# Kernel optimization log

Hardware: AMD Instinct MI355X
Metric: run time of the kernel (lower is better)

## Reference

```python
import jax, jax.numpy as jnp
import numpy as np


def setup_inputs() -> dict:
    key = jax.random.key(0)
    k1, k2 = jax.random.split(key)
    bg = jax.random.normal(k1, (1, 4, 32, 32, 32, 16), dtype=jnp.float32)
    gm = jax.random.uniform(k2, (1, 1, 128, 128, 128), dtype=jnp.float32)
    return {"bg": bg, "gm": gm}


def _prep(coord, size):
    # replicate boundary: clamp sample coords into [0, size-1]
    coord = jnp.clip(coord, 0.0, float(size - 1))
    i0f = jnp.floor(coord)
    frac = coord - i0f
    i0 = i0f.astype(jnp.int32)
    i1 = jnp.minimum(i0 + 1, size - 1)
    return i0, i1, frac


def reference(bg, gm):
    # bg: (n,c,h,w,d,up) 4D bilateral grid; gm: (n,1,gh,gw,gd) guidance volume
    n, c, h, w, d, up = bg.shape
    _, _, gh, gw, gd = gm.shape
    f32 = jnp.float32

    # voxel-space sample coordinates (module: hg/(h_img-1) * (h-1) etc.)
    x = jnp.arange(gh, dtype=f32) * (f32(h - 1) / f32(gh - 1))  # (gh,)
    y = jnp.arange(gw, dtype=f32) * (f32(w - 1) / f32(gw - 1))  # (gw,)
    z = jnp.arange(gd, dtype=f32) * (f32(d - 1) / f32(gd - 1))  # (gd,)
    t = gm[:, 0] * f32(up - 1)                                   # (n,gh,gw,gd)

    x0, x1, fx = _prep(x, h)
    y0, y1, fy = _prep(y, w)
    z0, z1, fz = _prep(z, d)
    t0, t1, ft = _prep(t, up)

    def opts(i0, i1, frac, shape):
        i0 = i0.reshape(shape); i1 = i1.reshape(shape); frac = frac.reshape(shape)
        return [(i0, 1.0 - frac), (i1, frac)]

    xo = opts(x0, x1, fx, (1, gh, 1, 1))
    yo = opts(y0, y1, fy, (1, 1, gw, 1))
    zo = opts(z0, z1, fz, (1, 1, 1, gd))
    to = [(t0, 1.0 - ft), (t1, ft)]  # already (n,gh,gw,gd)

    bidx = jnp.arange(n)[:, None, None, None]        # (n,1,1,1)
    bgc = jnp.moveaxis(bg, 1, -1)                    # (n,h,w,d,up,c)

    acc = jnp.zeros((n, gh, gw, gd, c), dtype=bg.dtype)
    # 2^4 = 16 corners of quadri-linear interpolation (grid_pull order=1)
    for ix, wx in xo:
        for iy, wy in yo:
            for iz, wz in zo:
                for it, wt in to:
                    vals = bgc[bidx, ix, iy, iz, it]         # (n,gh,gw,gd,c)
                    wgt = (wx * wy * wz * wt)[..., None]     # (n,gh,gw,gd,1)
                    acc = acc + vals * wgt
    return jnp.moveaxis(acc, -1, 1)                  # (n,c,gh,gw,gd)
```

## Files before the change

kernel.cpp:

```cpp
#include <hip/hip_runtime.h>
#include <hip/hip_fp16.h>


#define S_ (31.0f / 127.0f)
#define CH_STRIDE 524288
#define TOTAL 2097152

#define NX 4
#define NY 4
#define NZ 10
#define NNODES (NX * NY * NZ)
#define NODE_DW 68
#define LDS_DW (NNODES * NODE_DW)

#define PK(x, y) __builtin_bit_cast(float, __floats2half2_rn((x), (y)))
#define H2(f) __builtin_bit_cast(__half2, f)

typedef float vf4 __attribute__((ext_vector_type(4)));

__device__ __forceinline__ void nt_store4(float* p, float a, float b, float c, float d) {
    vf4 v; v.x = a; v.y = b; v.z = c; v.w = d;
    __builtin_nontemporal_store(v, (vf4*)p);
}

__global__ __launch_bounds__(512, 6) void bgrid_slice_v14(
    const float* __restrict__ bg,
    const float* __restrict__ gm,
    float* __restrict__ out)
{
    __shared__ __align__(16) float lds[LDS_DW];

    const int tid = threadIdx.x;
    const int b = blockIdx.x;
    const int tile = ((b & 7) << 7) + (b >> 3);
    const int bk = tile & 3;
    const int bj = (tile >> 2) & 15;
    const int bi = tile >> 6;

    const int i0 = bi * 8, j0 = bj * 8, k0 = bk * 32;
    const int x_base = (int)((float)i0 * S_);
    const int y_base = (int)((float)j0 * S_);
    const int z_base = (int)((float)k0 * S_);

    const int kq = tid & 7;
    const int lj = (tid >> 3) & 7;
    const int li = tid >> 6;
    const int i = i0 + li, j = j0 + lj;
    const int kk = k0 + (kq << 2);
    const int idx = (i << 14) | (j << 7) | kk;
    const vf4 g4v = __builtin_nontemporal_load((const vf4*)&gm[idx]);
    float4 g4; g4.x = g4v.x; g4.y = g4v.y; g4.z = g4v.z; g4.w = g4v.w;

    #pragma unroll
    for (int it = 0; it < 2; ++it) {
        const int q = tid + (it << 9);
        if (q < 640) {
            const int s4 = q & 3;
            const int node = q >> 2;
            const int a = node / 40;
            const int rem = node - a * 40;
            const int bb = rem / 10;
            const int cz = rem - bb * 10;
            const int gx = min(x_base + a, 31);
            const int gy = min(y_base + bb, 31);
            const int gz = min(z_base + cz, 31);
            const int gbase = (((gx * 32 + gy) * 32 + gz) << 4) + (s4 << 2);

            const float4 L0 = *(const float4*)&bg[gbase];
            const float4 L1 = *(const float4*)&bg[gbase + CH_STRIDE];
            const float4 L2 = *(const float4*)&bg[gbase + 2 * CH_STRIDE];
            const float4 L3 = *(const float4*)&bg[gbase + 3 * CH_STRIDE];

            float2 p0, p1, p2, p3;
            p0.x = PK(L0.x, L1.x); p0.y = PK(L2.x, L3.x);
            p1.x = PK(L0.y, L1.y); p1.y = PK(L2.y, L3.y);
            p2.x = PK(L0.z, L1.z); p2.y = PK(L2.z, L3.z);
            p3.x = PK(L0.w, L1.w); p3.y = PK(L2.w, L3.w);

            const int s0 = node * NODE_DW + (s4 << 4);
            float4 w;
            w.x = p0.x; w.y = p0.y; w.z = p1.x; w.w = p1.y;
            *(float4*)&lds[s0] = w;
            w.x = p1.x; w.y = p1.y; w.z = p2.x; w.w = p2.y;
            *(float4*)&lds[s0 + 4] = w;
            w.x = p2.x; w.y = p2.y; w.z = p3.x; w.w = p3.y;
            *(float4*)&lds[s0 + 8] = w;
            if (s4 < 3) *(float2*)&lds[s0 + 12] = p3;
            if (s4 > 0) *(float2*)&lds[s0 - 2]  = p0;
        }
    }
    __syncthreads();

    const float xf = fminf((float)i * S_, 31.0f);
    const float yf = fminf((float)j * S_, 31.0f);
    const int x0g = (int)xf; const float fx = xf - (float)x0g;
    const int y0g = (int)yf; const float fy = yf - (float)y0g;
    const int xi0 = x0g - x_base, xi1 = min(x0g + 1, 31) - x_base;
    const int yi0 = y0g - y_base, yi1 = min(y0g + 1, 31) - y_base;

    const int AX0 = xi0 * (NY * NZ * NODE_DW);
    const int AX1 = xi1 * (NY * NZ * NODE_DW);
    const int BY0 = yi0 * (NZ * NODE_DW);
    const int BY1 = yi1 * (NZ * NODE_DW);

    const float wx1 = fx, wx0 = 1.0f - fx;
    const float wy1 = fy, wy0 = 1.0f - fy;
    const __half2 W00 = __float2half2_rn(wx0 * wy0);
    const __half2 W01 = __float2half2_rn(wx0 * wy1);
    const __half2 W10 = __float2half2_rn(wx1 * wy0);
    const __half2 W11 = __float2half2_rn(wx1 * wy1);

    float o0[4], o1[4], o2[4], o3[4];

#pragma unroll
    for (int v = 0; v < 4; ++v) {
        const float g = (v == 0) ? g4.x : (v == 1) ? g4.y : (v == 2) ? g4.z : g4.w;
        float t = fminf(fmaxf(g * 15.0f, 0.0f), 15.0f);
        const int t0 = min((int)t, 14);
        const float ft = t - (float)t0;
        const __half2 ft2 = __float2half2_rn(ft);

        const float zf = fminf((float)(kk + v) * S_, 31.0f);
        const int z0g = (int)zf;
        const float fz = zf - (float)z0g;
        const int zi0 = z0g - z_base;
        const int zi1 = min(z0g + 1, 31) - z_base;
        const __half2 fz2 = __float2half2_rn(fz);

        const int CZ0 = zi0 * NODE_DW + (t0 << 2);
        const int CZ1 = zi1 * NODE_DW + (t0 << 2);

        const float4 a00 = *(const float4*)&lds[AX0 + BY0 + CZ0];
        const float4 a01 = *(const float4*)&lds[AX0 + BY1 + CZ0];
        const float4 a10 = *(const float4*)&lds[AX1 + BY0 + CZ0];
        const float4 a11 = *(const float4*)&lds[AX1 + BY1 + CZ0];
        const float4 b00 = *(const float4*)&lds[AX0 + BY0 + CZ1];
        const float4 b01 = *(const float4*)&lds[AX0 + BY1 + CZ1];
        const float4 b10 = *(const float4*)&lds[AX1 + BY0 + CZ1];
        const float4 b11 = *(const float4*)&lds[AX1 + BY1 + CZ1];

        __half2 Plo01 = __hmul2(W00, H2(a00.x));
        __half2 Plo23 = __hmul2(W00, H2(a00.y));
        __half2 Phi01 = __hmul2(W00, H2(a00.z));
        __half2 Phi23 = __hmul2(W00, H2(a00.w));
        Plo01 = __hfma2(W01, H2(a01.x), Plo01);
        Plo23 = __hfma2(W01, H2(a01.y), Plo23);
        Phi01 = __hfma2(W01, H2(a01.z), Phi01);
        Phi23 = __hfma2(W01, H2(a01.w), Phi23);
        Plo01 = __hfma2(W10, H2(a10.x), Plo01);
        Plo23 = __hfma2(W10, H2(a10.y), Plo23);
        Phi01 = __hfma2(W10, H2(a10.z), Phi01);
        Phi23 = __hfma2(W10, H2(a10.w), Phi23);
        Plo01 = __hfma2(W11, H2(a11.x), Plo01);
        Plo23 = __hfma2(W11, H2(a11.y), Plo23);
        Phi01 = __hfma2(W11, H2(a11.z), Phi01);
        Phi23 = __hfma2(W11, H2(a11.w), Phi23);

        __half2 Qlo01 = __hmul2(W00, H2(b00.x));
        __half2 Qlo23 = __hmul2(W00, H2(b00.y));
        __half2 Qhi01 = __hmul2(W00, H2(b00.z));
        __half2 Qhi23 = __hmul2(W00, H2(b00.w));
        Qlo01 = __hfma2(W01, H2(b01.x), Qlo01);
        Qlo23 = __hfma2(W01, H2(b01.y), Qlo23);
        Qhi01 = __hfma2(W01, H2(b01.z), Qhi01);
        Qhi23 = __hfma2(W01, H2(b01.w), Qhi23);
        Qlo01 = __hfma2(W10, H2(b10.x), Qlo01);
        Qlo23 = __hfma2(W10, H2(b10.y), Qlo23);
        Qhi01 = __hfma2(W10, H2(b10.z), Qhi01);
        Qhi23 = __hfma2(W10, H2(b10.w), Qhi23);
        Qlo01 = __hfma2(W11, H2(b11.x), Qlo01);
        Qlo23 = __hfma2(W11, H2(b11.y), Qlo23);
        Qhi01 = __hfma2(W11, H2(b11.z), Qhi01);
        Qhi23 = __hfma2(W11, H2(b11.w), Qhi23);

        const __half2 Rlo01 = __hfma2(fz2, __hsub2(Qlo01, Plo01), Plo01);
        const __half2 Rlo23 = __hfma2(fz2, __hsub2(Qlo23, Plo23), Plo23);
        const __half2 Rhi01 = __hfma2(fz2, __hsub2(Qhi01, Phi01), Phi01);
        const __half2 Rhi23 = __hfma2(fz2, __hsub2(Qhi23, Phi23), Phi23);

        const __half2 r01 = __hfma2(ft2, __hsub2(Rhi01, Rlo01), Rlo01);
        const __half2 r23 = __hfma2(ft2, __hsub2(Rhi23, Rlo23), Rlo23);

        o0[v] = __low2float(r01);
        o1[v] = __high2float(r01);
        o2[v] = __low2float(r23);
        o3[v] = __high2float(r23);
    }

    nt_store4(&out[idx],             o0[0], o0[1], o0[2], o0[3]);
    nt_store4(&out[idx + TOTAL],     o1[0], o1[1], o1[2], o1[3]);
    nt_store4(&out[idx + 2 * TOTAL], o2[0], o2[1], o2[2], o2[3]);
    nt_store4(&out[idx + 3 * TOTAL], o3[0], o3[1], o3[2], o3[3]);
}

extern "C" void kernel_launch(void* const* d_in, const int* in_sizes, int n_in,
                              void* d_out, int out_size, void* d_ws, size_t ws_size,
                              hipStream_t stream) {
    const float* bg = (const float*)d_in[0];
    const float* gm = (const float*)d_in[1];
    float* out = (float*)d_out;

    dim3 grid(1024);
    dim3 block(512);
    bgrid_slice_v14<<<grid, block, 0, stream>>>(bg, gm, out);
}
```

Before: 16.57 us.

## Pre-interpolate along x during LDS staging to halve per-voxel gathers

Instead of staging raw 4x4x10 grid nodes, the staging phase now performs the x-direction lerp in fp32 for each of the 8 output rows of the tile and stores 8 x-collapsed planes in LDS. The per-voxel inner loop then needs only 4 corner reads (y,z) instead of 8 and does a bilinear instead of trilinear blend in half2. This cuts LDS reads and half2 FMAs in the hot loop. In exchange the staging phase issues twice as many global loads, runs more iterations and uses more LDS. It also drops the overlapping duplicate-t layout, so each corner now takes two float2 reads.

```diff
diff --git a/kernel.cpp b/kernel.cpp
--- a/kernel.cpp
+++ b/kernel.cpp
@@ -6,12 +6,13 @@
 #define CH_STRIDE 524288
 #define TOTAL 2097152
 
-#define NX 4
 #define NY 4
 #define NZ 10
-#define NNODES (NX * NY * NZ)
-#define NODE_DW 68
-#define LDS_DW (NNODES * NODE_DW)
+#define NODE_DW 36
+#define NPLANES (8 * NY * NZ)
+#define LDS_DW (NPLANES * NODE_DW)
+#define IS (NY * NZ * NODE_DW)
+#define YS (NZ * NODE_DW)
 
 #define PK(x, y) __builtin_bit_cast(float, __floats2half2_rn((x), (y)))
 #define H2(f) __builtin_bit_cast(__half2, f)
@@ -23,7 +24,7 @@
     __builtin_nontemporal_store(v, (vf4*)p);
 }
 
-__global__ __launch_bounds__(512, 6) void bgrid_slice_v14(
+__global__ __launch_bounds__(512, 6) void bgrid_slice_v15(
     const float* __restrict__ bg,
     const float* __restrict__ gm,
     float* __restrict__ out)
@@ -38,7 +39,6 @@
     const int bi = tile >> 6;
 
     const int i0 = bi * 8, j0 = bj * 8, k0 = bk * 32;
-    const int x_base = (int)((float)i0 * S_);
     const int y_base = (int)((float)j0 * S_);
     const int z_base = (int)((float)k0 * S_);
 
@@ -52,63 +52,65 @@
     float4 g4; g4.x = g4v.x; g4.y = g4v.y; g4.z = g4v.z; g4.w = g4v.w;
 
     #pragma unroll
-    for (int it = 0; it < 2; ++it) {
+    for (int it = 0; it < 3; ++it) {
         const int q = tid + (it << 9);
-        if (q < 640) {
-            const int s4 = q & 3;
-            const int node = q >> 2;
-            const int a = node / 40;
-            const int rem = node - a * 40;
-            const int bb = rem / 10;
-            const int cz = rem - bb * 10;
-            const int gx = min(x_base + a, 31);
-            const int gy = min(y_base + bb, 31);
-            const int gz = min(z_base + cz, 31);
-            const int gbase = (((gx * 32 + gy) * 32 + gz) << 4) + (s4 << 2);
+        if (q < 1280) {
+            const int i_loc = q & 7;
+            const int r = q >> 3;
+            const int seg = r & 3;
+            const int yz = r >> 2;
+            const int y = yz / 10;
+            const int z = yz - y * 10;
 
-            const float4 L0 = *(const float4*)&bg[gbase];
-            const float4 L1 = *(const float4*)&bg[gbase + CH_STRIDE];
-            const float4 L2 = *(const float4*)&bg[gbase + 2 * CH_STRIDE];
-            const float4 L3 = *(const float4*)&bg[gbase + 3 * CH_STRIDE];
+            const float xf = fminf((float)(i0 + i_loc) * S_, 31.0f);
+            const int x0g = (int)xf;
+            const float fx = xf - (float)x0g;
+            const int x1g = min(x0g + 1, 31);
+            const int gy = min(y_base + y, 31);
+            const int gz = min(z_base + z, 31);
+            const int a0 = (((x0g * 32 + gy) * 32 + gz) << 4) + (seg << 2);
+            const int a1 = (((x1g * 32 + gy) * 32 + gz) << 4) + (seg << 2);
 
-            float2 p0, p1, p2, p3;
-            p0.x = PK(L0.x, L1.x); p0.y = PK(L2.x, L3.x);
-            p1.x = PK(L0.y, L1.y); p1.y = PK(L2.y, L3.y);
-            p2.x = PK(L0.z, L1.z); p2.y = PK(L2.z, L3.z);
-            p3.x = PK(L0.w, L1.w); p3.y = PK(L2.w, L3.w);
+            const float4 A0 = *(const float4*)&bg[a0];
+            const float4 A1 = *(const float4*)&bg[a0 + CH_STRIDE];
+            const float4 A2 = *(const float4*)&bg[a0 + 2 * CH_STRIDE];
+            const float4 A3 = *(const float4*)&bg[a0 + 3 * CH_STRIDE];
+            const float4 B0 = *(const float4*)&bg[a1];
+            const float4 B1 = *(const float4*)&bg[a1 + CH_STRIDE];
+            const float4 B2 = *(const float4*)&bg[a1 + 2 * CH_STRIDE];
+            const float4 B3 = *(const float4*)&bg[a1 + 3 * CH_STRIDE];
 
-            const int s0 = node * NODE_DW + (s4 << 4);
-            float4 w;
-            w.x = p0.x; w.y = p0.y; w.z = p1.x; w.w = p1.y;
-            *(float4*)&lds[s0] = w;
-            w.x = p1.x; w.y = p1.y; w.z = p2.x; w.w = p2.y;
-            *(float4*)&lds[s0 + 4] = w;
-            w.x = p2.x; w.y = p2.y; w.z = p3.x; w.w = p3.y;
-            *(float4*)&lds[s0 + 8] = w;
-            if (s4 < 3) *(float2*)&lds[s0 + 12] = p3;
-            if (s4 > 0) *(float2*)&lds[s0 - 2]  = p0;
+            float4 C0, C1, C2, C3;
+            C0.x = fmaf(fx, B0.x - A0.x, A0.x); C0.y = fmaf(fx, B0.y - A0.y, A0.y);
+            C0.z = fmaf(fx, B0.z - A0.z, A0.z); C0.w = fmaf(fx, B0.w - A0.w, A0.w);
+            C1.x = fmaf(fx, B1.x - A1.x, A1.x); C1.y = fmaf(fx, B1.y - A1.y, A1.y);
+            C1.z = fmaf(fx, B1.z - A1.z, A1.z); C1.w = fmaf(fx, B1.w - A1.w, A1.w);
+            C2.x = fmaf(fx, B2.x - A2.x, A2.x); C2.y = fmaf(fx, B2.y - A2.y, A2.y);
+            C2.z = fmaf(fx, B2.z - A2.z, A2.z); C2.w = fmaf(fx, B2.w - A2.w, A2.w);
+            C3.x = fmaf(fx, B3.x - A3.x, A3.x); C3.y = fmaf(fx, B3.y - A3.y, A3.y);
+            C3.z = fmaf(fx, B3.z - A3.z, A3.z); C3.w = fmaf(fx, B3.w - A3.w, A3.w);
+
+            float4 W0, W1;
+            W0.x = PK(C0.x, C1.x); W0.y = PK(C2.x, C3.x);
+            W0.z = PK(C0.y, C1.y); W0.w = PK(C2.y, C3.y);
+            W1.x = PK(C0.z, C1.z); W1.y = PK(C2.z, C3.z);
+            W1.z = PK(C0.w, C1.w); W1.w = PK(C2.w, C3.w);
+
+            const int d = ((i_loc * NY + y) * NZ + z) * NODE_DW + (seg << 3);
+            *(float4*)&lds[d] = W0;
+            *(float4*)&lds[d + 4] = W1;
         }
     }
     __syncthreads();
 
-    const float xf = fminf((float)i * S_, 31.0f);
     const float yf = fminf((float)j * S_, 31.0f);
-    const int x0g = (int)xf; const float fx = xf - (float)x0g;
     const int y0g = (int)yf; const float fy = yf - (float)y0g;
-    const int xi0 = x0g - x_base, xi1 = min(x0g + 1, 31) - x_base;
-    const int yi0 = y0g - y_base, yi1 = min(y0g + 1, 31) - y_base;
+    const int BY0 = (y0g - y_base) * YS;
+    const int BY1 = (min(y0g + 1, 31) - y_base) * YS;
+    const int PI = li * IS;
 
-    const int AX0 = xi0 * (NY * NZ * NODE_DW);
-    const int AX1 = xi1 * (NY * NZ * NODE_DW);
-    const int BY0 = yi0 * (NZ * NODE_DW);
-    const int BY1 = yi1 * (NZ * NODE_DW);
-
-    const float wx1 = fx, wx0 = 1.0f - fx;
-    const float wy1 = fy, wy0 = 1.0f - fy;
-    const __half2 W00 = __float2half2_rn(wx0 * wy0);
-    const __half2 W01 = __float2half2_rn(wx0 * wy1);
-    const __half2 W10 = __float2half2_rn(wx1 * wy0);
-    const __half2 W11 = __float2half2_rn(wx1 * wy1);
+    const __half2 Wy0 = __float2half2_rn(1.0f - fy);
+    const __half2 Wy1 = __float2half2_rn(fy);
 
     float o0[4], o1[4], o2[4], o3[4];
 
@@ -127,59 +129,43 @@
         const int zi1 = min(z0g + 1, 31) - z_base;
         const __half2 fz2 = __float2half2_rn(fz);
 
-        const int CZ0 = zi0 * NODE_DW + (t0 << 2);
-        const int CZ1 = zi1 * NODE_DW + (t0 << 2);
+        const int CZ0 = zi0 * NODE_DW + (t0 << 1);
+        const int CZ1 = zi1 * NODE_DW + (t0 << 1);
 
-        const float4 a00 = *(const float4*)&lds[AX0 + BY0 + CZ0];
-        const float4 a01 = *(const float4*)&lds[AX0 + BY1 + CZ0];
-        const float4 a10 = *(const float4*)&lds[AX1 + BY0 + CZ0];
-        const float4 a11 = *(const float4*)&lds[AX1 + BY1 + CZ0];
-        const float4 b00 = *(const float4*)&lds[AX0 + BY0 + CZ1];
-        const float4 b01 = *(const float4*)&lds[AX0 + BY1 + CZ1];
-        const float4 b10 = *(const float4*)&lds[AX1 + BY0 + CZ1];
-        const float4 b11 = *(const float4*)&lds[AX1 + BY1 + CZ1];
+        const float2 c00lo = *(const float2*)&lds[PI + BY0 + CZ0];
+        const float2 c00hi = *(const float2*)&lds[PI + BY0 + CZ0 + 2];
+        const float2 c01lo = *(const float2*)&lds[PI + BY1 + CZ0];
+        const float2 c01hi = *(const float2*)&lds[PI + BY1 + CZ0 + 2];
+        const float2 c10lo = *(const float2*)&lds[PI + BY0 + CZ1];
+        const float2 c10hi = *(const float2*)&lds[PI + BY0 + CZ1 + 2];
+        const float2 c11lo = *(const float2*)&lds[PI + BY1 + CZ1];
+        const float2 c11hi = *(const float2*)&lds[PI + BY1 + CZ1 + 2];
 
-        __half2 Plo01 = __hmul2(W00, H2(a00.x));
-        __half2 Plo23 = __hmul2(W00, H2(a00.y));
-        __half2 Phi01 = __hmul2(W00, H2(a00.z));
-        __half2 Phi23 = __hmul2(W00, H2(a00.w));
-        Plo01 = __hfma2(W01, H2(a01.x), Plo01);
-        Plo23 = __hfma2(W01, H2(a01.y), Plo23);
-        Phi01 = __hfma2(W01, H2(a01.z), Phi01);
-        Phi23 = __hfma2(W01, H2(a01.w), Phi23);
-        Plo01 = __hfma2(W10, H2(a10.x), Plo01);
-        Plo23 = __hfma2(W10, H2(a10.y), Plo23);
-        Phi01 = __hfma2(W10, H2(a10.z), Phi01);
-        Phi23 = __hfma2(W10, H2(a10.w), Phi23);
-        Plo01 = __hfma2(W11, H2(a11.x), Plo01);
-        Plo23 = __hfma2(W11, H2(a11.y), Plo23);
-        Phi01 = __hfma2(W11, H2(a11.z), Phi01);
-        Phi23 = __hfma2(W11, H2(a11.w), Phi23);
+        __half2 L01 = __hmul2(Wy0, H2(c00lo.x));
+        __half2 L23 = __hmul2(Wy0, H2(c00lo.y));
+        __half2 Lh01 = __hmul2(Wy0, H2(c00hi.x));
+        __half2 Lh23 = __hmul2(Wy0, H2(c00hi.y));
+        L01 = __hfma2(Wy1, H2(c01lo.x), L01);
+        L23 = __hfma2(Wy1, H2(c01lo.y), L23);
+        Lh01 = __hfma2(Wy1, H2(c01hi.x), Lh01);
+        Lh23 = __hfma2(Wy1, H2(c01hi.y), Lh23);
 
-        __half2 Qlo01 = __hmul2(W00, H2(b00.x));
-        __half2 Qlo23 = __hmul2(W00, H2(b00.y));
-        __half2 Qhi01 = __hmul2(W00, H2(b00.z));
-        __half2 Qhi23 = __hmul2(W00, H2(b00.w));
-        Qlo01 = __hfma2(W01, H2(b01.x), Qlo01);
-        Qlo23 = __hfma2(W01, H2(b01.y), Qlo23);
-        Qhi01 = __hfma2(W01, H2(b01.z), Qhi01);
-        Qhi23 = __hfma2(W01, H2(b01.w), Qhi23);
-        Qlo01 = __hfma2(W10, H2(b10.x), Qlo01);
-        Qlo23 = __hfma2(W10, H2(b10.y), Qlo23);
-        Qhi01 = __hfma2(W10, H2(b10.z), Qhi01);
-        Qhi23 = __hfma2(W10, H2(b10.w), Qhi23);
-        Qlo01 = __hfma2(W11, H2(b11.x), Qlo01);
-        Qlo23 = __hfma2(W11, H2(b11.y), Qlo23);
-        Qhi01 = __hfma2(W11, H2(b11.z), Qhi01);
-        Qhi23 = __hfma2(W11, H2(b11.w), Qhi23);
+        __half2 M01 = __hmul2(Wy0, H2(c10lo.x));
+        __half2 M23 = __hmul2(Wy0, H2(c10lo.y));
+        __half2 Mh01 = __hmul2(Wy0, H2(c10hi.x));
+        __half2 Mh23 = __hmul2(Wy0, H2(c10hi.y));
+        M01 = __hfma2(Wy1, H2(c11lo.x), M01);
+        M23 = __hfma2(Wy1, H2(c11lo.y), M23);
+        Mh01 = __hfma2(Wy1, H2(c11hi.x), Mh01);
+        Mh23 = __hfma2(Wy1, H2(c11hi.y), Mh23);
 
-        const __half2 Rlo01 = __hfma2(fz2, __hsub2(Qlo01, Plo01), Plo01);
-        const __half2 Rlo23 = __hfma2(fz2, __hsub2(Qlo23, Plo23), Plo23);
-        const __half2 Rhi01 = __hfma2(fz2, __hsub2(Qhi01, Phi01), Phi01);
-        const __half2 Rhi23 = __hfma2(fz2, __hsub2(Qhi23, Phi23), Phi23);
+        const __half2 R01 = __hfma2(fz2, __hsub2(M01, L01), L01);
+        const __half2 R23 = __hfma2(fz2, __hsub2(M23, L23), L23);
+        const __half2 Rh01 = __hfma2(fz2, __hsub2(Mh01, Lh01), Lh01);
+        const __half2 Rh23 = __hfma2(fz2, __hsub2(Mh23, Lh23), Lh23);
 
-        const __half2 r01 = __hfma2(ft2, __hsub2(Rhi01, Rlo01), Rlo01);
-        const __half2 r23 = __hfma2(ft2, __hsub2(Rhi23, Rlo23), Rlo23);
+        const __half2 r01 = __hfma2(ft2, __hsub2(Rh01, R01), R01);
+        const __half2 r23 = __hfma2(ft2, __hsub2(Rh23, R23), R23);
 
         o0[v] = __low2float(r01);
         o1[v] = __high2float(r01);
@@ -202,5 +188,5 @@
 
     dim3 grid(1024);
     dim3 block(512);
-    bgrid_slice_v14<<<grid, block, 0, stream>>>(bg, gm, out);
+    bgrid_slice_v15<<<grid, block, 0, stream>>>(bg, gm, out);
 }
```

New measurement: 20.52 us. +23.8%, slower.
